# Kernel tuning notes

Measured on AMD Instinct MI355X. Metric: run time of the kernel, lower is better.

The kernel has to match this reference:

```python
import jax, jax.numpy as jnp
import numpy as np

N = 50000        # nodes
E = 800000       # edges
H = 128          # in = hidden = out width
L = 4            # num_layers
BN_EPS = 1e-5


def _bn(x, g, b):
    # training-mode batch norm over the node dimension (biased variance, as torch)
    mu = jnp.mean(x, axis=0)
    var = jnp.mean((x - mu) ** 2, axis=0)
    return (x - mu) * jax.lax.rsqrt(var + BN_EPS) * g + b


def setup_inputs() -> dict:
    key = jax.random.key(0)
    ks = jax.random.split(key, 16)
    s = 0.05
    return {
        "x": jax.random.normal(ks[0], (N, H), dtype=jnp.float32),
        "edge_index": jax.random.randint(ks[1], (2, E), 0, N, dtype=jnp.int32),
        # stacked per-layer MLP params (all layers share dims H->H->H)
        "fc1_w": jax.random.normal(ks[2], (L, H, H), dtype=jnp.float32) * s,
        "fc1_b": jnp.zeros((L, H), dtype=jnp.float32),
        "bn1_g": jnp.ones((L, H), dtype=jnp.float32),
        "bn1_b": jnp.zeros((L, H), dtype=jnp.float32),
        "fc2_w": jax.random.normal(ks[3], (L, H, H), dtype=jnp.float32) * s,
        "fc2_b": jnp.zeros((L, H), dtype=jnp.float32),
        "bn2_g": jnp.ones((L, H), dtype=jnp.float32),
        "bn2_b": jnp.zeros((L, H), dtype=jnp.float32),
        # outer per-layer BatchNorm (intended one-per-GIN-layer)
        "bn3_g": jnp.ones((L, H), dtype=jnp.float32),
        "bn3_b": jnp.zeros((L, H), dtype=jnp.float32),
        # final classifier
        "fc_w": jax.random.normal(ks[4], (H, H), dtype=jnp.float32) * s,
        "fc_b": jnp.zeros((H,), dtype=jnp.float32),
    }


def reference(x, edge_index, fc1_w, fc1_b, bn1_g, bn1_b, fc2_w, fc2_b,
              bn2_g, bn2_b, bn3_g, bn3_b, fc_w, fc_b):
    src = edge_index[0]
    dst = edge_index[1]
    for i in range(L):
        # GINConv, eps=0: h = MLP((1+eps)*x + sum_{j in N(v)} x_j)
        agg = jax.ops.segment_sum(x[src], dst, num_segments=N)  # [N, H]
        h = x + agg
        # MLP: relu(bn1(fc1(h))) -> bn2(fc2(.))
        h = jax.nn.relu(_bn(h @ fc1_w[i].T + fc1_b[i], bn1_g[i], bn1_b[i]))
        h = _bn(h @ fc2_w[i].T + fc2_b[i], bn2_g[i], bn2_b[i])
        # outer BN + ReLU per layer
        x = jax.nn.relu(_bn(h, bn3_g[i], bn3_b[i]))
    return x @ fc_w.T + fc_b  # [N, H]
```

## Files before the change

### kernel.cpp

```cpp
#include <hip/hip_runtime.h>

#define NN 50000
#define HD 128
#define NL 4
#define BN_EPS 1e-5f
#define NTILES 3125
#define MAXDEG 64

typedef __attribute__((ext_vector_type(8))) short short8;
typedef __attribute__((ext_vector_type(4))) float f32x4;
typedef __attribute__((ext_vector_type(4))) uint uint4v;

__device__ inline ushort f2bf(float f){
  uint u = __float_as_uint(f);
  uint r = (u + 0x7fffu + ((u >> 16) & 1u)) >> 16;
  return (ushort)r;
}
__device__ inline float bflo(uint u){ return __uint_as_float(u << 16); }
__device__ inline float bfhi(uint u){ return __uint_as_float(u & 0xffff0000u); }
__device__ inline uint pk2(float lo, float hi){
  return (uint)f2bf(lo) | ((uint)f2bf(hi) << 16);
}

__global__ __launch_bounds__(256) void cast_all(const float* __restrict__ x,
                                                const float* __restrict__ w1,
                                                const float* __restrict__ w2,
                                                const float* __restrict__ wf,
                                                ushort* __restrict__ xb,
                                                ushort* __restrict__ wb){
  const int NX = NN * HD / 4;
  const int NT = NX + 36864;
  int i = blockIdx.x * 256 + threadIdx.x;
  int stride = gridDim.x * 256;
  for (; i < NT; i += stride){
    const float* src; ushort* dst;
    if (i < NX){ src = x + i * 4; dst = xb + i * 4; }
    else {
      int k = i - NX;
      dst = wb + k * 4;
      if (k < 16384)      src = w1 + k * 4;
      else if (k < 32768) src = w2 + (k - 16384) * 4;
      else                src = wf + (k - 32768) * 4;
    }
    float4 v = *(const float4*)src;
    ushort4 r;
    r.x = f2bf(v.x); r.y = f2bf(v.y); r.z = f2bf(v.z); r.w = f2bf(v.w);
    *(ushort4*)dst = r;
  }
}

__global__ void fill1_kernel(const int* __restrict__ dst, int* __restrict__ cnt,
                             int* __restrict__ pos, int E){
  int e = (blockIdx.x * 256 + threadIdx.x) * 4;
  if (e + 4 <= E){
    int4 d = *(const int4*)(dst + e);
    int4 p;
    p.x = atomicAdd(&cnt[d.x], 1);
    p.y = atomicAdd(&cnt[d.y], 1);
    p.z = atomicAdd(&cnt[d.z], 1);
    p.w = atomicAdd(&cnt[d.w], 1);
    *(int4*)(pos + e) = p;
  } else {
    for (; e < E; ++e) pos[e] = atomicAdd(&cnt[dst[e]], 1);
  }
}

__global__ void fill2_kernel(const int* __restrict__ src, const int* __restrict__ dst,
                             const int* __restrict__ pos, int* __restrict__ slots, int E){
  int e = (blockIdx.x * 256 + threadIdx.x) * 4;
  if (e + 4 <= E){
    int4 d = *(const int4*)(dst + e);
    int4 p = *(const int4*)(pos + e);
    int4 s = *(const int4*)(src + e);
    slots[d.x * MAXDEG + p.x] = s.x;
    slots[d.y * MAXDEG + p.y] = s.y;
    slots[d.z * MAXDEG + p.z] = s.z;
    slots[d.w * MAXDEG + p.w] = s.w;
  } else {
    for (; e < E; ++e) slots[dst[e] * MAXDEG + pos[e]] = src[e];
  }
}

__device__ inline void bn_params8(const float* __restrict__ st, const float* __restrict__ gA,
                                  const float* __restrict__ gB, const float* __restrict__ bB,
                                  int mode, float* sS, float* sT){
  int c = threadIdx.x;
  if (c < 128){
    float s0 = 0.f, s1 = 0.f;
#pragma unroll
    for (int k = 0; k < 8; ++k){
      s0 += st[k * 256 + c];
      s1 += st[k * 256 + 128 + c];
    }
    const float invN = 1.f / (float)NN;
    float mu = s0 * invN;
    float var = fmaxf(s1 * invN - mu * mu, 0.f);
    float S, T;
    if (mode == 0){
      S = gA[c] * rsqrtf(var + BN_EPS);
      T = gB[c] - mu * S;
    } else {
      float inv2 = rsqrtf(var + BN_EPS);
      float tt = gA[c] * inv2;
      float inv3 = rsqrtf(tt * tt * var + BN_EPS);
      S = tt * inv3 * gB[c];
      T = bB[c] - mu * S;
    }
    sS[c] = S; sT[c] = T;
  }
}

template<bool AFF>
__global__ __launch_bounds__(512, 4) void aggemm_t(const ushort* __restrict__ xin,
                                                   const int* __restrict__ deg,
                                                   const int* __restrict__ slots,
                                                   const ushort* __restrict__ W,
                                                   const float* __restrict__ bias,
                                                   ushort* __restrict__ Yb,
                                                   float* __restrict__ statsOut,
                                                   const float* __restrict__ statsIn,
                                                   const float* __restrict__ g2,
                                                   const float* __restrict__ g3,
                                                   const float* __restrict__ b3){
  __shared__ uint4v w4[128 * 17];
  __shared__ uint4v a4[8][16 * 17];
  __shared__ float ssum[128];
  __shared__ float ssq[128];
  __shared__ float sS[128];
  __shared__ float sT[128];

  const uint4v* Wg = (const uint4v*)W;
  for (int c = threadIdx.x; c < 2048; c += 512){
    w4[(c >> 4) * 17 + (c & 15)] = Wg[c];
  }
  if (AFF) bn_params8(statsIn, g2, g3, b3, 1, sS, sT);
  if (threadIdx.x < 128){ ssum[threadIdx.x] = 0.f; ssq[threadIdx.x] = 0.f; }
  __syncthreads();

  int wave = threadIdx.x >> 6;
  int lane = threadIdx.x & 63;
  int grp  = lane >> 4;
  int col  = lane & 15;
  int tile = blockIdx.x * 8 + wave;
  bool tv = tile < NTILES;

  float S[8], T[8];
  if (AFF){
#pragma unroll
    for (int k = 0; k < 8; ++k){ S[k] = sS[col * 8 + k]; T[k] = sT[col * 8 + k]; }
  }

  const uint4v* x4 = (const uint4v*)xin;

#define ACC8(v)                                                                 \
  if (AFF){                                                                     \
    a[0]+=fmaxf(bflo((v).x)*S[0]+T[0],0.f); a[1]+=fmaxf(bfhi((v).x)*S[1]+T[1],0.f); \
    a[2]+=fmaxf(bflo((v).y)*S[2]+T[2],0.f); a[3]+=fmaxf(bfhi((v).y)*S[3]+T[3],0.f); \
    a[4]+=fmaxf(bflo((v).z)*S[4]+T[4],0.f); a[5]+=fmaxf(bfhi((v).z)*S[5]+T[5],0.f); \
    a[6]+=fmaxf(bflo((v).w)*S[6]+T[6],0.f); a[7]+=fmaxf(bfhi((v).w)*S[7]+T[7],0.f); \
  } else {                                                                      \
    a[0]+=bflo((v).x); a[1]+=bfhi((v).x); a[2]+=bflo((v).y); a[3]+=bfhi((v).y); \
    a[4]+=bflo((v).z); a[5]+=bfhi((v).z); a[6]+=bflo((v).w); a[7]+=bfhi((v).w); \
  }

  if (tv){
    for (int it = 0; it < 4; ++it){
      int node = tile * 16 + it * 4 + grp;
      int e = deg[node];
      const int* sl = slots + node * MAXDEG;
      float a[8];
      {
        uint4v v = x4[node * 16 + col];
        if (AFF){
          a[0]=fmaxf(bflo(v.x)*S[0]+T[0],0.f); a[1]=fmaxf(bfhi(v.x)*S[1]+T[1],0.f);
          a[2]=fmaxf(bflo(v.y)*S[2]+T[2],0.f); a[3]=fmaxf(bfhi(v.y)*S[3]+T[3],0.f);
          a[4]=fmaxf(bflo(v.z)*S[4]+T[4],0.f); a[5]=fmaxf(bfhi(v.z)*S[5]+T[5],0.f);
          a[6]=fmaxf(bflo(v.w)*S[6]+T[6],0.f); a[7]=fmaxf(bfhi(v.w)*S[7]+T[7],0.f);
        } else {
          a[0]=bflo(v.x); a[1]=bfhi(v.x); a[2]=bflo(v.y); a[3]=bfhi(v.y);
          a[4]=bflo(v.z); a[5]=bfhi(v.z); a[6]=bflo(v.w); a[7]=bfhi(v.w);
        }
      }
      int j = 0;
      for (; j + 8 <= e; j += 8){
        int i0 = sl[j+0], i1 = sl[j+1], i2 = sl[j+2], i3 = sl[j+3];
        int i4 = sl[j+4], i5 = sl[j+5], i6 = sl[j+6], i7 = sl[j+7];
        uint4v v0 = x4[i0 * 16 + col];
        uint4v v1 = x4[i1 * 16 + col];
        uint4v v2 = x4[i2 * 16 + col];
        uint4v v3 = x4[i3 * 16 + col];
        uint4v v4 = x4[i4 * 16 + col];
        uint4v v5 = x4[i5 * 16 + col];
        uint4v v6 = x4[i6 * 16 + col];
        uint4v v7 = x4[i7 * 16 + col];
        ACC8(v0); ACC8(v1); ACC8(v2); ACC8(v3);
        ACC8(v4); ACC8(v5); ACC8(v6); ACC8(v7);
      }
      for (; j + 4 <= e; j += 4){
        int i0 = sl[j+0], i1 = sl[j+1], i2 = sl[j+2], i3 = sl[j+3];
        uint4v v0 = x4[i0 * 16 + col];
        uint4v v1 = x4[i1 * 16 + col];
        uint4v v2 = x4[i2 * 16 + col];
        uint4v v3 = x4[i3 * 16 + col];
        ACC8(v0); ACC8(v1); ACC8(v2); ACC8(v3);
      }
      for (; j < e; ++j){
        uint4v v = x4[sl[j] * 16 + col];
        ACC8(v);
      }
      uint4v o;
      o.x = pk2(a[0], a[1]); o.y = pk2(a[2], a[3]);
      o.z = pk2(a[4], a[5]); o.w = pk2(a[6], a[7]);
      a4[wave][(it * 4 + grp) * 17 + col] = o;
    }
  }
#undef ACC8
  __syncthreads();

  int m = lane & 15, q = lane >> 4;
  f32x4 acc[8];
#pragma unroll
  for (int i = 0; i < 8; ++i) acc[i] = (f32x4)0.f;

#pragma unroll
  for (int kt = 0; kt < 4; ++kt){
    uint4v t = a4[wave][m * 17 + kt * 4 + q];
    short8 af = *(short8*)&t;
#pragma unroll
    for (int to = 0; to < 8; ++to){
      uint4v bw = w4[(to * 16 + m) * 17 + kt * 4 + q];
      acc[to] = __builtin_amdgcn_mfma_f32_16x16x32_bf16(af, *(short8*)&bw, acc[to], 0, 0, 0);
    }
  }

#pragma unroll
  for (int to = 0; to < 8; ++to){
    int colo = to * 16 + m;
    float bc = bias[colo];
    float ls = 0.f, lq = 0.f;
    if (tv){
#pragma unroll
      for (int r = 0; r < 4; ++r){
        float v = acc[to][r] + bc;
        int row = tile * 16 + q * 4 + r;
        __builtin_nontemporal_store(__builtin_bit_cast(ushort, f2bf(v)), Yb + row * 128 + colo);
        ls += v; lq += v * v;
      }
    }
    ls += __shfl_xor(ls, 16); lq += __shfl_xor(lq, 16);
    ls += __shfl_xor(ls, 32); lq += __shfl_xor(lq, 32);
    if (tv && q == 0){ atomicAdd(&ssum[colo], ls); atomicAdd(&ssq[colo], lq); }
  }
  __syncthreads();
  if (threadIdx.x < 128){
    int sb = (blockIdx.x & 7) * 256;
    atomicAdd(&statsOut[sb + threadIdx.x], ssum[threadIdx.x]);
    atomicAdd(&statsOut[sb + 128 + threadIdx.x], ssq[threadIdx.x]);
  }
}

__global__ __launch_bounds__(512) void gemm_kernel(const ushort* __restrict__ A,
                                                   const ushort* __restrict__ W,
                                                   const float* __restrict__ bias,
                                                   ushort* __restrict__ Yb,
                                                   float* __restrict__ Yf,
                                                   float* __restrict__ statsOut,
                                                   const float* __restrict__ statsIn,
                                                   const float* __restrict__ gA,
                                                   const float* __restrict__ gB,
                                                   const float* __restrict__ bB,
                                                   int mode){
  __shared__ uint4v w4[128 * 17];
  __shared__ float ssum[128];
  __shared__ float ssq[128];
  __shared__ float sS[128];
  __shared__ float sT[128];
  const uint4v* Wg = (const uint4v*)W;
  for (int c = threadIdx.x; c < 2048; c += 512){
    w4[(c >> 4) * 17 + (c & 15)] = Wg[c];
  }
  if (statsIn) bn_params8(statsIn, gA, gB, bB, mode, sS, sT);
  if (threadIdx.x < 128){ ssum[threadIdx.x] = 0.f; ssq[threadIdx.x] = 0.f; }
  __syncthreads();

  int wave = threadIdx.x >> 6;
  int lane = threadIdx.x & 63;
  int m = lane & 15, q = lane >> 4;
  int tile = blockIdx.x * 8 + wave;
  bool tv = tile < NTILES;
  const uint4v* A4 = (const uint4v*)A;

  f32x4 acc[8];
#pragma unroll
  for (int i = 0; i < 8; ++i) acc[i] = (f32x4)0.f;

#pragma unroll
  for (int kt = 0; kt < 4; ++kt){
    short8 af = (short8)0;
    if (tv){
      uint4v t = __builtin_nontemporal_load(A4 + (tile * 16 + m) * 16 + kt * 4 + q);
      if (statsIn){
        int kc = kt * 32 + q * 8;
        uint4v pk;
        pk.x = pk2(fmaxf(bflo(t.x)*sS[kc+0]+sT[kc+0],0.f),
                   fmaxf(bfhi(t.x)*sS[kc+1]+sT[kc+1],0.f));
        pk.y = pk2(fmaxf(bflo(t.y)*sS[kc+2]+sT[kc+2],0.f),
                   fmaxf(bfhi(t.y)*sS[kc+3]+sT[kc+3],0.f));
        pk.z = pk2(fmaxf(bflo(t.z)*sS[kc+4]+sT[kc+4],0.f),
                   fmaxf(bfhi(t.z)*sS[kc+5]+sT[kc+5],0.f));
        pk.w = pk2(fmaxf(bflo(t.w)*sS[kc+6]+sT[kc+6],0.f),
                   fmaxf(bfhi(t.w)*sS[kc+7]+sT[kc+7],0.f));
        t = pk;
      }
      af = *(short8*)&t;
    }
#pragma unroll
    for (int to = 0; to < 8; ++to){
      uint4v bw = w4[(to * 16 + m) * 17 + kt * 4 + q];
      acc[to] = __builtin_amdgcn_mfma_f32_16x16x32_bf16(af, *(short8*)&bw, acc[to], 0, 0, 0);
    }
  }

  bool dost = (statsOut != nullptr);
#pragma unroll
  for (int to = 0; to < 8; ++to){
    int col = to * 16 + m;
    float bc = bias[col];
    float ls = 0.f, lq = 0.f;
    if (tv){
#pragma unroll
      for (int r = 0; r < 4; ++r){
        float v = acc[to][r] + bc;
        int row = tile * 16 + q * 4 + r;
        if (Yb) __builtin_nontemporal_store(__builtin_bit_cast(ushort, f2bf(v)), Yb + row * 128 + col);
        else    __builtin_nontemporal_store(v, Yf + row * 128 + col);
        ls += v; lq += v * v;
      }
    }
    if (dost){
      ls += __shfl_xor(ls, 16); lq += __shfl_xor(lq, 16);
      ls += __shfl_xor(ls, 32); lq += __shfl_xor(lq, 32);
      if (tv && q == 0){ atomicAdd(&ssum[col], ls); atomicAdd(&ssq[col], lq); }
    }
  }
  if (dost){
    __syncthreads();
    if (threadIdx.x < 128){
      int sb = (blockIdx.x & 7) * 256;
      atomicAdd(&statsOut[sb + threadIdx.x], ssum[threadIdx.x]);
      atomicAdd(&statsOut[sb + 128 + threadIdx.x], ssq[threadIdx.x]);
    }
  }
}

extern "C" void kernel_launch(void* const* d_in, const int* in_sizes, int n_in,
                              void* d_out, int out_size, void* d_ws, size_t ws_size,
                              hipStream_t stream) {
  const float* x     = (const float*)d_in[0];
  const int*   ei    = (const int*)d_in[1];
  const float* fc1_w = (const float*)d_in[2];
  const float* fc1_b = (const float*)d_in[3];
  const float* bn1_g = (const float*)d_in[4];
  const float* bn1_b = (const float*)d_in[5];
  const float* fc2_w = (const float*)d_in[6];
  const float* fc2_b = (const float*)d_in[7];
  const float* bn2_g = (const float*)d_in[8];
  const float* bn3_g = (const float*)d_in[10];
  const float* bn3_b = (const float*)d_in[11];
  const float* fc_w  = (const float*)d_in[12];
  const float* fc_b  = (const float*)d_in[13];

  int E = in_sizes[1] / 2;
  const int* srcp = ei;
  const int* dstp = ei + E;

  char* ws = (char*)d_ws;
  int*    cnt    = (int*)(ws + 0);
  float*  stats  = (float*)(ws + 200064);
  int*    pos    = (int*)(ws + 265600);
  int*    slots  = (int*)(ws + 3465600);
  ushort* wb     = (ushort*)(ws + 16265600);
  ushort* xb     = (ushort*)(ws + 16560512);
  ushort* y1b    = (ushort*)(ws + 29360512);
  ushort* y2b    = (ushort*)(ws + 42160512);

  hipMemsetAsync(ws, 0, 265600, stream);

  cast_all<<<2048, 256, 0, stream>>>(x, fc1_w, fc2_w, fc_w, xb, wb);

  const int EB4 = (E / 4 + 255) / 256 + 1;
  fill1_kernel<<<EB4, 256, 0, stream>>>(dstp, cnt, pos, E);
  fill2_kernel<<<EB4, 256, 0, stream>>>(srcp, dstp, pos, slots, E);

  const int gb = (NTILES + 7) / 8;

  for (int i = 0; i < NL; ++i){
    if (i == 0){
      aggemm_t<false><<<gb, 512, 0, stream>>>(xb, cnt, slots, wb + i * 16384,
                                              fc1_b + i * 128, y1b,
                                              stats + (i * 2) * 2048,
                                              nullptr, nullptr, nullptr, nullptr);
    } else {
      aggemm_t<true><<<gb, 512, 0, stream>>>(y2b, cnt, slots, wb + i * 16384,
                                             fc1_b + i * 128, y1b,
                                             stats + (i * 2) * 2048,
                                             stats + ((i - 1) * 2 + 1) * 2048,
                                             bn2_g + (i - 1) * 128,
                                             bn3_g + (i - 1) * 128,
                                             bn3_b + (i - 1) * 128);
    }
    gemm_kernel<<<gb, 512, 0, stream>>>(y1b, wb + 65536 + i * 16384, fc2_b + i * 128,
                                        y2b, nullptr, stats + (i * 2 + 1) * 2048,
                                        stats + (i * 2) * 2048, bn1_g + i * 128,
                                        bn1_b + i * 128, nullptr, 0);
  }

  gemm_kernel<<<gb, 512, 0, stream>>>(y2b, wb + 131072, fc_b,
                                      nullptr, (float*)d_out, nullptr,
                                      stats + 7 * 2048, bn2_g + 384,
                                      bn3_g + 384, bn3_b + 384, 1);
}
```

Baseline: 425.5 us.

## Split tiles across waves in aggregate-GEMM and GEMM kernels for more parallelism

The aggregation kernel now gives each wave one group of 4 nodes instead of a whole 16-node tile, so each block covers 2 tiles and four waves share each tile. Each wave then computes 2 of the 8 output column blocks. The plain GEMM kernel similarly splits each tile's output columns across two waves, with 4 tiles per block. Grid sizes grow and occupancy hints rise. The aim is to cut per-wave serial gather latency and register pressure, at the cost of more blocks, more reloads of the weight tile into shared memory, and more stats atomics.

```diff
diff --git a/kernel.cpp b/kernel.cpp
--- a/kernel.cpp
+++ b/kernel.cpp
@@ -111,7 +111,7 @@
 }
 
 template<bool AFF>
-__global__ __launch_bounds__(512, 4) void aggemm_t(const ushort* __restrict__ xin,
+__global__ __launch_bounds__(512, 6) void aggemm_t(const ushort* __restrict__ xin,
                                                    const int* __restrict__ deg,
                                                    const int* __restrict__ slots,
                                                    const ushort* __restrict__ W,
@@ -123,7 +123,7 @@
                                                    const float* __restrict__ g3,
                                                    const float* __restrict__ b3){
   __shared__ uint4v w4[128 * 17];
-  __shared__ uint4v a4[8][16 * 17];
+  __shared__ uint4v a4[2][16 * 17];
   __shared__ float ssum[128];
   __shared__ float ssq[128];
   __shared__ float sS[128];
@@ -139,9 +139,11 @@
 
   int wave = threadIdx.x >> 6;
   int lane = threadIdx.x & 63;
+  int tl   = wave >> 2;
+  int qd   = wave & 3;
   int grp  = lane >> 4;
   int col  = lane & 15;
-  int tile = blockIdx.x * 8 + wave;
+  int tile = blockIdx.x * 2 + tl;
   bool tv = tile < NTILES;
 
   float S[8], T[8];
@@ -164,84 +166,82 @@
   }
 
   if (tv){
-    for (int it = 0; it < 4; ++it){
-      int node = tile * 16 + it * 4 + grp;
-      int e = deg[node];
-      const int* sl = slots + node * MAXDEG;
-      float a[8];
-      {
-        uint4v v = x4[node * 16 + col];
-        if (AFF){
-          a[0]=fmaxf(bflo(v.x)*S[0]+T[0],0.f); a[1]=fmaxf(bfhi(v.x)*S[1]+T[1],0.f);
-          a[2]=fmaxf(bflo(v.y)*S[2]+T[2],0.f); a[3]=fmaxf(bfhi(v.y)*S[3]+T[3],0.f);
-          a[4]=fmaxf(bflo(v.z)*S[4]+T[4],0.f); a[5]=fmaxf(bfhi(v.z)*S[5]+T[5],0.f);
-          a[6]=fmaxf(bflo(v.w)*S[6]+T[6],0.f); a[7]=fmaxf(bfhi(v.w)*S[7]+T[7],0.f);
-        } else {
-          a[0]=bflo(v.x); a[1]=bfhi(v.x); a[2]=bflo(v.y); a[3]=bfhi(v.y);
-          a[4]=bflo(v.z); a[5]=bfhi(v.z); a[6]=bflo(v.w); a[7]=bfhi(v.w);
-        }
+    int node = tile * 16 + qd * 4 + grp;
+    int e = deg[node];
+    const int* sl = slots + node * MAXDEG;
+    float a[8];
+    {
+      uint4v v = x4[node * 16 + col];
+      if (AFF){
+        a[0]=fmaxf(bflo(v.x)*S[0]+T[0],0.f); a[1]=fmaxf(bfhi(v.x)*S[1]+T[1],0.f);
+        a[2]=fmaxf(bflo(v.y)*S[2]+T[2],0.f); a[3]=fmaxf(bfhi(v.y)*S[3]+T[3],0.f);
+        a[4]=fmaxf(bflo(v.z)*S[4]+T[4],0.f); a[5]=fmaxf(bfhi(v.z)*S[5]+T[5],0.f);
+        a[6]=fmaxf(bflo(v.w)*S[6]+T[6],0.f); a[7]=fmaxf(bfhi(v.w)*S[7]+T[7],0.f);
+      } else {
+        a[0]=bflo(v.x); a[1]=bfhi(v.x); a[2]=bflo(v.y); a[3]=bfhi(v.y);
+        a[4]=bflo(v.z); a[5]=bfhi(v.z); a[6]=bflo(v.w); a[7]=bfhi(v.w);
       }
-      int j = 0;
-      for (; j + 8 <= e; j += 8){
-        int i0 = sl[j+0], i1 = sl[j+1], i2 = sl[j+2], i3 = sl[j+3];
-        int i4 = sl[j+4], i5 = sl[j+5], i6 = sl[j+6], i7 = sl[j+7];
-        uint4v v0 = x4[i0 * 16 + col];
-        uint4v v1 = x4[i1 * 16 + col];
-        uint4v v2 = x4[i2 * 16 + col];
-        uint4v v3 = x4[i3 * 16 + col];
-        uint4v v4 = x4[i4 * 16 + col];
-        uint4v v5 = x4[i5 * 16 + col];
-        uint4v v6 = x4[i6 * 16 + col];
-        uint4v v7 = x4[i7 * 16 + col];
-        ACC8(v0); ACC8(v1); ACC8(v2); ACC8(v3);
-        ACC8(v4); ACC8(v5); ACC8(v6); ACC8(v7);
-      }
-      for (; j + 4 <= e; j += 4){
-        int i0 = sl[j+0], i1 = sl[j+1], i2 = sl[j+2], i3 = sl[j+3];
-        uint4v v0 = x4[i0 * 16 + col];
-        uint4v v1 = x4[i1 * 16 + col];
-        uint4v v2 = x4[i2 * 16 + col];
-        uint4v v3 = x4[i3 * 16 + col];
-        ACC8(v0); ACC8(v1); ACC8(v2); ACC8(v3);
-      }
-      for (; j < e; ++j){
-        uint4v v = x4[sl[j] * 16 + col];
-        ACC8(v);
-      }
-      uint4v o;
-      o.x = pk2(a[0], a[1]); o.y = pk2(a[2], a[3]);
-      o.z = pk2(a[4], a[5]); o.w = pk2(a[6], a[7]);
-      a4[wave][(it * 4 + grp) * 17 + col] = o;
-    }
+    }
+    int j = 0;
+    for (; j + 8 <= e; j += 8){
+      int i0 = sl[j+0], i1 = sl[j+1], i2 = sl[j+2], i3 = sl[j+3];
+      int i4 = sl[j+4], i5 = sl[j+5], i6 = sl[j+6], i7 = sl[j+7];
+      uint4v v0 = x4[i0 * 16 + col];
+      uint4v v1 = x4[i1 * 16 + col];
+      uint4v v2 = x4[i2 * 16 + col];
+      uint4v v3 = x4[i3 * 16 + col];
+      uint4v v4 = x4[i4 * 16 + col];
+      uint4v v5 = x4[i5 * 16 + col];
+      uint4v v6 = x4[i6 * 16 + col];
+      uint4v v7 = x4[i7 * 16 + col];
+      ACC8(v0); ACC8(v1); ACC8(v2); ACC8(v3);
+      ACC8(v4); ACC8(v5); ACC8(v6); ACC8(v7);
+    }
+    for (; j + 4 <= e; j += 4){
+      int i0 = sl[j+0], i1 = sl[j+1], i2 = sl[j+2], i3 = sl[j+3];
+      uint4v v0 = x4[i0 * 16 + col];
+      uint4v v1 = x4[i1 * 16 + col];
+      uint4v v2 = x4[i2 * 16 + col];
+      uint4v v3 = x4[i3 * 16 + col];
+      ACC8(v0); ACC8(v1); ACC8(v2); ACC8(v3);
+    }
+    for (; j < e; ++j){
+      uint4v v = x4[sl[j] * 16 + col];
+      ACC8(v);
+    }
+    uint4v o;
+    o.x = pk2(a[0], a[1]); o.y = pk2(a[2], a[3]);
+    o.z = pk2(a[4], a[5]); o.w = pk2(a[6], a[7]);
+    a4[tl][(qd * 4 + grp) * 17 + col] = o;
   }
 #undef ACC8
   __syncthreads();
 
   int m = lane & 15, q = lane >> 4;
-  f32x4 acc[8];
-#pragma unroll
-  for (int i = 0; i < 8; ++i) acc[i] = (f32x4)0.f;
+  f32x4 acc[2];
+  acc[0] = (f32x4)0.f; acc[1] = (f32x4)0.f;
 
 #pragma unroll
   for (int kt = 0; kt < 4; ++kt){
-    uint4v t = a4[wave][m * 17 + kt * 4 + q];
+    uint4v t = a4[tl][m * 17 + kt * 4 + q];
     short8 af = *(short8*)&t;
 #pragma unroll
-    for (int to = 0; to < 8; ++to){
+    for (int t2 = 0; t2 < 2; ++t2){
+      int to = qd * 2 + t2;
       uint4v bw = w4[(to * 16 + m) * 17 + kt * 4 + q];
-      acc[to] = __builtin_amdgcn_mfma_f32_16x16x32_bf16(af, *(short8*)&bw, acc[to], 0, 0, 0);
-    }
-  }
-
-#pragma unroll
-  for (int to = 0; to < 8; ++to){
-    int colo = to * 16 + m;
+      acc[t2] = __builtin_amdgcn_mfma_f32_16x16x32_bf16(af, *(short8*)&bw, acc[t2], 0, 0, 0);
+    }
+  }
+
+#pragma unroll
+  for (int t2 = 0; t2 < 2; ++t2){
+    int colo = (qd * 2 + t2) * 16 + m;
     float bc = bias[colo];
     float ls = 0.f, lq = 0.f;
     if (tv){
 #pragma unroll
       for (int r = 0; r < 4; ++r){
-        float v = acc[to][r] + bc;
+        float v = acc[t2][r] + bc;
         int row = tile * 16 + q * 4 + r;
         __builtin_nontemporal_store(__builtin_bit_cast(ushort, f2bf(v)), Yb + row * 128 + colo);
         ls += v; lq += v * v;
@@ -259,7 +259,7 @@
   }
 }
 
-__global__ __launch_bounds__(512) void gemm_kernel(const ushort* __restrict__ A,
+__global__ __launch_bounds__(512, 8) void gemm_kernel(const ushort* __restrict__ A,
                                                    const ushort* __restrict__ W,
                                                    const float* __restrict__ bias,
                                                    ushort* __restrict__ Yb,
@@ -286,13 +286,15 @@
   int wave = threadIdx.x >> 6;
   int lane = threadIdx.x & 63;
   int m = lane & 15, q = lane >> 4;
-  int tile = blockIdx.x * 8 + wave;
+  int tl   = wave >> 1;
+  int half = wave & 1;
+  int tile = blockIdx.x * 4 + tl;
   bool tv = tile < NTILES;
   const uint4v* A4 = (const uint4v*)A;
 
-  f32x4 acc[8];
-#pragma unroll
-  for (int i = 0; i < 8; ++i) acc[i] = (f32x4)0.f;
+  f32x4 acc[4];
+#pragma unroll
+  for (int i = 0; i < 4; ++i) acc[i] = (f32x4)0.f;
 
 #pragma unroll
   for (int kt = 0; kt < 4; ++kt){
@@ -315,22 +317,23 @@
       af = *(short8*)&t;
     }
 #pragma unroll
-    for (int to = 0; to < 8; ++to){
+    for (int t4 = 0; t4 < 4; ++t4){
+      int to = half * 4 + t4;
       uint4v bw = w4[(to * 16 + m) * 17 + kt * 4 + q];
-      acc[to] = __builtin_amdgcn_mfma_f32_16x16x32_bf16(af, *(short8*)&bw, acc[to], 0, 0, 0);
+      acc[t4] = __builtin_amdgcn_mfma_f32_16x16x32_bf16(af, *(short8*)&bw, acc[t4], 0, 0, 0);
     }
   }
 
   bool dost = (statsOut != nullptr);
 #pragma unroll
-  for (int to = 0; to < 8; ++to){
-    int col = to * 16 + m;
+  for (int t4 = 0; t4 < 4; ++t4){
+    int col = (half * 4 + t4) * 16 + m;
     float bc = bias[col];
     float ls = 0.f, lq = 0.f;
     if (tv){
 #pragma unroll
       for (int r = 0; r < 4; ++r){
-        float v = acc[to][r] + bc;
+        float v = acc[t4][r] + bc;
         int row = tile * 16 + q * 4 + r;
         if (Yb) __builtin_nontemporal_store(__builtin_bit_cast(ushort, f2bf(v)), Yb + row * 128 + col);
         else    __builtin_nontemporal_store(v, Yf + row * 128 + col);
@@ -392,16 +395,17 @@
   fill1_kernel<<<EB4, 256, 0, stream>>>(dstp, cnt, pos, E);
   fill2_kernel<<<EB4, 256, 0, stream>>>(srcp, dstp, pos, slots, E);
 
-  const int gb = (NTILES + 7) / 8;
+  const int ga = (NTILES + 1) / 2;
+  const int gb = (NTILES + 3) / 4;
 
   for (int i = 0; i < NL; ++i){
     if (i == 0){
-      aggemm_t<false><<<gb, 512, 0, stream>>>(xb, cnt, slots, wb + i * 16384,
+      aggemm_t<false><<<ga, 512, 0, stream>>>(xb, cnt, slots, wb + i * 16384,
                                               fc1_b + i * 128, y1b,
                                               stats + (i * 2) * 2048,
                                               nullptr, nullptr, nullptr, nullptr);
     } else {
-      aggemm_t<true><<<gb, 512, 0, stream>>>(y2b, cnt, slots, wb + i * 16384,
+      aggemm_t<true><<<ga, 512, 0, stream>>>(y2b, cnt, slots, wb + i * 16384,
                                              fc1_b + i * 128, y1b,
                                              stats + (i * 2) * 2048,
                                              stats + ((i - 1) * 2 + 1) * 2048,
```

Result: slower. 467.7 us (+9.9%).
